# Optimization experiments

Measured on AMD Instinct MI355X. Metric: run time of the kernel, lower is better.

## Reference

```python
import jax, jax.numpy as jnp
import numpy as np

NUM_HEADS = 8

B, N, M = 2, 10000, 320000
QD = KD = HD = 256


def setup_inputs() -> dict:
    key = jax.random.key(0)
    k1, k2, k3, k4, k5 = jax.random.split(key, 5)
    x_q = jax.random.normal(k1, (B, N, QD), dtype=jnp.float32)
    x_k = jax.random.normal(k2, (B, N, KD), dtype=jnp.float32)
    mask = jax.random.randint(k3, (2, M), 0, N, dtype=jnp.int64)
    # xavier_uniform: limit = sqrt(6/(fan_in+fan_out))
    lim_q = float(np.sqrt(6.0 / (QD + HD)))
    lim_k = float(np.sqrt(6.0 / (KD + HD)))
    w_q = jax.random.uniform(k4, (QD, HD), minval=-lim_q, maxval=lim_q, dtype=jnp.float32)
    w_k = jax.random.uniform(k5, (KD, HD), minval=-lim_k, maxval=lim_k, dtype=jnp.float32)
    return {"x_q": x_q, "x_k": x_k, "mask": mask, "w_q": w_q, "w_k": w_k}


def reference(x_q, x_k, mask, w_q, w_k):
    b, n, _ = x_q.shape
    m = mask.shape[1]
    d = w_q.shape[1]          # hidden_dim
    h = NUM_HEADS
    dh = d // h
    q = x_q @ w_q             # (b, n, d)
    k = x_k @ w_k             # (b, n, d)
    # edge gather + elementwise multiply
    prod = q[:, mask[0], :] * k[:, mask[1], :]            # (b, m, d)
    # head buffer is i // (d/h): contiguous blocks -> reshape-sum
    a = prod.reshape(b, m, h, dh).sum(axis=-1)            # (b, m, h)
    a = a / jnp.sqrt(jnp.float32(w_k.shape[0]))           # / sqrt(key_dim)
    # segment softmax over destination index = mask[1 - reduce_dim], reduce_dim=1 -> mask[0]
    idx = mask[0]
    a = a - a.max()                                       # global max, as in source
    e = jnp.exp(a)                                        # (b, m, h)
    seg = jnp.zeros((b, n, h), e.dtype).at[:, idx, :].add(e)
    return e / (seg[:, idx, :] + 1e-16)
```

## Files before the change

kernel.cpp:

```cpp
#include <hip/hip_runtime.h>
#include <hip/hip_bf16.h>
#include <hip/hip_fp16.h>

#define DHID 256
#define NHEAD 8
#define BATCH 2
#define PAD 96

typedef _Float16 h8 __attribute__((ext_vector_type(8)));
typedef _Float16 h2 __attribute__((ext_vector_type(2)));
typedef float f4 __attribute__((ext_vector_type(4)));
typedef int i2 __attribute__((ext_vector_type(2)));

__global__ __launch_bounds__(256) void prep_kernel(
    const float* __restrict__ Wq, const float* __restrict__ Wk,
    _Float16* __restrict__ Wfq, _Float16* __restrict__ Wfk,
    int* __restrict__ cnt, int N)
{
    if (blockIdx.z == 2) {
        const int gid = (blockIdx.y * 8 + blockIdx.x) * 256
                      + threadIdx.y * 32 + threadIdx.x;
        if (gid < N) cnt[gid] = 0;
        return;
    }
    const float* W = blockIdx.z ? Wk : Wq;
    _Float16* Wf   = blockIdx.z ? Wfk : Wfq;
    __shared__ float tile[32][33];
    const int tx = threadIdx.x;
    const int ty = threadIdx.y;
    const int n0 = blockIdx.x * 32;
    const int k0 = blockIdx.y * 32;
#pragma unroll
    for (int j = 0; j < 32; j += 8)
        tile[ty + j][tx] = W[(size_t)(k0 + ty + j) * DHID + n0 + tx];
    __syncthreads();
#pragma unroll
    for (int j = 0; j < 32; j += 8) {
        const int n = n0 + ty + j;
        const int k = k0 + tx;
        const size_t u = ((size_t)(n >> 4) * 32 + (k >> 3)) * 16 + (n & 15);
        Wf[u * 8 + (k & 7)] = (_Float16)tile[tx][ty + j];
    }
}

__global__ __launch_bounds__(256, 4) void gemm_mfma(
    const float* __restrict__ Xq, const float* __restrict__ Xk,
    const _Float16* __restrict__ Wfq, const _Float16* __restrict__ Wfk,
    _Float16* __restrict__ Qh, _Float16* __restrict__ Kh,
    const int* __restrict__ mask, int* __restrict__ cnt, int* __restrict__ sde,
    int nx, int Mrows, int M, int N)
{
    const int t = threadIdx.x;
    if ((int)blockIdx.x >= nx) {
        const int sb = ((int)blockIdx.x - nx) + (blockIdx.z ? 64 : 0);
        for (int e = sb * 256 + t; e < M; e += 128 * 256) {
            int s = mask[e];
            int r = atomicAdd(&cnt[s], 1);
            if (r < PAD) {
                i2 v; v[0] = mask[M + e]; v[1] = e;
                *(i2*)(sde + ((size_t)s * PAD + r) * 2) = v;
            }
        }
        return;
    }

    const float* X     = blockIdx.z ? Xk : Xq;
    const _Float16* Wf = blockIdx.z ? Wfk : Wfq;
    _Float16* C        = blockIdx.z ? Kh : Qh;

    const int lane = t & 63;
    const int wave = t >> 6;
    const int quad = lane >> 4;
    const int l16  = lane & 15;
    const int rowBase = blockIdx.x * 64;
    int arow = rowBase + wave * 16 + l16;
    if (arow >= Mrows) arow = Mrows - 1;

    h8 af[8];
#pragma unroll
    for (int kc = 0; kc < 8; ++kc) {
        const float* p = X + (size_t)arow * DHID + (kc * 4 + quad) * 8;
        f4 v0 = *(const f4*)p;
        f4 v1 = *(const f4*)(p + 4);
        h8 hv;
        hv[0]=(_Float16)v0[0]; hv[1]=(_Float16)v0[1]; hv[2]=(_Float16)v0[2]; hv[3]=(_Float16)v0[3];
        hv[4]=(_Float16)v1[0]; hv[5]=(_Float16)v1[1]; hv[6]=(_Float16)v1[2]; hv[7]=(_Float16)v1[3];
        af[kc] = hv;
    }

#pragma unroll 1
    for (int ct64 = 0; ct64 < 4; ++ct64) {
        f4 acc[4] = {{0,0,0,0},{0,0,0,0},{0,0,0,0},{0,0,0,0}};
#pragma unroll
        for (int kc = 0; kc < 8; ++kc) {
#pragma unroll
            for (int ct = 0; ct < 4; ++ct) {
                const h8 bf = *(const h8*)(Wf +
                    (((size_t)(ct64 * 4 + ct) * 32 + kc * 4 + quad) * 16 + l16) * 8);
                acc[ct] = __builtin_amdgcn_mfma_f32_16x16x32_f16(af[kc], bf, acc[ct], 0, 0, 0);
            }
        }
#pragma unroll
        for (int ct = 0; ct < 4; ++ct) {
#pragma unroll
            for (int r = 0; r < 4; ++r) {
                int grow = rowBase + wave * 16 + quad * 4 + r;
                if (grow < Mrows) {
                    int bb = grow >= N;
                    int nn = grow - (bb ? N : 0);
                    C[((size_t)nn * 2 + bb) * DHID + ct64 * 64 + ct * 16 + l16]
                        = (_Float16)acc[ct][r];
                }
            }
        }
    }
}

__global__ __launch_bounds__(256, 8) void edge_kernel(
    const _Float16* __restrict__ Qh, const _Float16* __restrict__ Kh,
    const int* __restrict__ cnt, const int* __restrict__ sde,
    float* __restrict__ out, int M, int N)
{
    __shared__ _Float16 evs[4][PAD][2][NHEAD];
    const int lane = threadIdx.x & 63;
    const int wave = threadIdx.x >> 6;
    const int c    = lane & 31;
    const int half = lane >> 5;
    const int h    = c >> 2;
    const int src  = blockIdx.x * 4 + wave;
    if (src >= N) return;
    int deg = cnt[src];
    if (deg > PAD) deg = PAD;
    if (deg == 0) return;
    const size_t base = (size_t)src * PAD;

    int dstv = 0, eidv = 0;
    if (lane < deg) {
        i2 v = *(const i2*)(sde + (base + lane) * 2);
        dstv = v[0]; eidv = v[1];
    }

    const _Float16* Qrow = Qh + (size_t)src * 2 * DHID;
    const h8 q0 = *(const h8*)(Qrow + c * 8);
    const h8 q1 = *(const h8*)(Qrow + DHID + c * 8);

    float seg0 = 0.f, seg1 = 0.f;
    for (int it = 0; it < deg; it += 8) {
        int pl[4], dd[4];
#pragma unroll
        for (int p = 0; p < 4; ++p) {
            pl[p] = it + p * 2 + half;
            if (it < 64) {
                dd[p] = __shfl(dstv, pl[p]);
            } else {
                int sc = pl[p] < deg ? pl[p] : deg - 1;
                dd[p] = sde[(base + sc) * 2];
            }
        }
        h8 k0v[4], k1v[4];
#pragma unroll
        for (int p = 0; p < 4; ++p) {
            const _Float16* Krow = Kh + (size_t)dd[p] * 2 * DHID;
            k0v[p] = *(const h8*)(Krow + c * 8);
            k1v[p] = *(const h8*)(Krow + DHID + c * 8);
        }
#pragma unroll
        for (int p = 0; p < 4; ++p) {
            float s0 = 0.f, s1 = 0.f;
#if __has_builtin(__builtin_amdgcn_fdot2)
#pragma unroll
            for (int u = 0; u < 4; ++u) {
                h2 a0, b0, a1, b1;
                a0[0] = q0[2*u];      a0[1] = q0[2*u+1];
                b0[0] = k0v[p][2*u];  b0[1] = k0v[p][2*u+1];
                a1[0] = q1[2*u];      a1[1] = q1[2*u+1];
                b1[0] = k1v[p][2*u];  b1[1] = k1v[p][2*u+1];
                s0 = __builtin_amdgcn_fdot2(a0, b0, s0, false);
                s1 = __builtin_amdgcn_fdot2(a1, b1, s1, false);
            }
#else
#pragma unroll
            for (int u = 0; u < 8; ++u) {
                s0 += (float)q0[u] * (float)k0v[p][u];
                s1 += (float)q1[u] * (float)k1v[p][u];
            }
#endif
            s0 += __shfl_xor(s0, 1); s0 += __shfl_xor(s0, 2);
            s1 += __shfl_xor(s1, 1); s1 += __shfl_xor(s1, 2);
            if ((c & 3) == 0 && pl[p] < deg) {
                _Float16 e0 = (_Float16)expf(s0 * 0.0625f);
                _Float16 e1 = (_Float16)expf(s1 * 0.0625f);
                evs[wave][pl[p]][0][h] = e0;
                evs[wave][pl[p]][1][h] = e1;
                seg0 += (float)e0; seg1 += (float)e1;
            }
        }
    }

    seg0 += __shfl_xor(seg0, 32);
    seg1 += __shfl_xor(seg1, 32);
    const float r0 = __builtin_amdgcn_rcpf(seg0 + 1e-16f);
    const float r1 = __builtin_amdgcn_rcpf(seg1 + 1e-16f);

    for (int it = 0; it < deg; it += 8) {
        int pl[4], ee[4];
#pragma unroll
        for (int p = 0; p < 4; ++p) {
            pl[p] = it + p * 2 + half;
            if (it < 64) {
                ee[p] = __shfl(eidv, pl[p]);
            } else {
                int sc = pl[p] < deg ? pl[p] : deg - 1;
                ee[p] = sde[(base + sc) * 2 + 1];
            }
        }
#pragma unroll
        for (int p = 0; p < 4; ++p) {
            if ((c & 3) == 0 && pl[p] < deg) {
                float v0 = (float)evs[wave][pl[p]][0][h] * r0;
                float v1 = (float)evs[wave][pl[p]][1][h] * r1;
                __builtin_nontemporal_store(v0, &out[(size_t)ee[p] * NHEAD + h]);
                __builtin_nontemporal_store(v1,
                    &out[(size_t)M * NHEAD + (size_t)ee[p] * NHEAD + h]);
            }
        }
    }
}

extern "C" void kernel_launch(void* const* d_in, const int* in_sizes, int n_in,
                              void* d_out, int out_size, void* d_ws, size_t ws_size,
                              hipStream_t stream) {
    const float* x_q  = (const float*)d_in[0];
    const float* x_k  = (const float*)d_in[1];
    const int*   mask = (const int*)d_in[2];
    const float* w_q  = (const float*)d_in[3];
    const float* w_k  = (const float*)d_in[4];
    float* out = (float*)d_out;

    const int M = in_sizes[2] / 2;
    const int N = in_sizes[0] / (BATCH * DHID);
    const int Mrows = BATCH * N;

    _Float16* Qh  = (_Float16*)d_ws;
    _Float16* Kh  = Qh  + (size_t)Mrows * DHID;
    _Float16* Wfq = Kh  + (size_t)Mrows * DHID;
    _Float16* Wfk = Wfq + (size_t)DHID * DHID;
    int*      cnt = (int*)(Wfk + (size_t)DHID * DHID);
    int*      sde = cnt + N;

    prep_kernel<<<dim3(DHID / 32, DHID / 32, 3), dim3(32, 8), 0, stream>>>(
        w_q, w_k, Wfq, Wfk, cnt, N);

    const int nx = (Mrows + 63) / 64;
    gemm_mfma<<<dim3(nx + 64, 1, 2), 256, 0, stream>>>(
        x_q, x_k, Wfq, Wfk, Qh, Kh, mask, cnt, sde, nx, Mrows, M, N);

    edge_kernel<<<dim3((N + 3) / 4), 256, 0, stream>>>(
        Qh, Kh, cnt, sde, out, M, N);
}
```

Before: 171.6 us.

## Stage swizzled weight tiles in LDS with double buffering in projection GEMM

```diff
diff --git a/kernel.cpp b/kernel.cpp
--- a/kernel.cpp
+++ b/kernel.cpp
@@ -38,12 +38,13 @@
     for (int j = 0; j < 32; j += 8) {
         const int n = n0 + ty + j;
         const int k = k0 + tx;
-        const size_t u = ((size_t)(n >> 4) * 32 + (k >> 3)) * 16 + (n & 15);
-        Wf[u * 8 + (k & 7)] = (_Float16)tile[tx][ty + j];
-    }
-}
-
-__global__ __launch_bounds__(256, 4) void gemm_mfma(
+        const int ct64 = n >> 6, nl = n & 63, c = k >> 3, jj = k & 7;
+        Wf[(size_t)ct64 * 16384 + nl * 256 + ((c ^ (nl & 7)) << 3) + jj]
+            = (_Float16)tile[tx][ty + j];
+    }
+}
+
+__global__ __launch_bounds__(256, 2) void gemm_mfma(
     const float* __restrict__ Xq, const float* __restrict__ Xk,
     const _Float16* __restrict__ Wfq, const _Float16* __restrict__ Wfk,
     _Float16* __restrict__ Qh, _Float16* __restrict__ Kh,
@@ -68,6 +69,8 @@
     const _Float16* Wf = blockIdx.z ? Wfk : Wfq;
     _Float16* C        = blockIdx.z ? Kh : Qh;
 
+    __shared__ _Float16 Bs[2][16384];
+
     const int lane = t & 63;
     const int wave = t >> 6;
     const int quad = lane >> 4;
@@ -75,6 +78,24 @@
     const int rowBase = blockIdx.x * 64;
     int arow = rowBase + wave * 16 + l16;
     if (arow >= Mrows) arow = Mrows - 1;
+
+    auto stageB = [&](int ct64, int buf) {
+#pragma unroll
+        for (int i = 0; i < 8; ++i) {
+            const int ci = i * 4 + wave;
+            const _Float16* src = Wf + (size_t)ct64 * 16384 + ci * 512 + lane * 8;
+            _Float16* dst = &Bs[buf][ci * 512];
+#if __has_builtin(__builtin_amdgcn_global_load_lds)
+            __builtin_amdgcn_global_load_lds(
+                (__attribute__((address_space(1))) void*)src,
+                (__attribute__((address_space(3))) void*)dst, 16, 0, 0);
+#else
+            *(h8*)(dst + lane * 8) = *(const h8*)src;
+#endif
+        }
+    };
+
+    stageB(0, 0);
 
     h8 af[8];
 #pragma unroll
@@ -88,18 +109,25 @@
         af[kc] = hv;
     }
 
-#pragma unroll 1
+    __syncthreads();
+
+#pragma unroll
     for (int ct64 = 0; ct64 < 4; ++ct64) {
+        const int cur = ct64 & 1;
+        if (ct64 < 3) stageB(ct64 + 1, cur ^ 1);
+
         f4 acc[4] = {{0,0,0,0},{0,0,0,0},{0,0,0,0},{0,0,0,0}};
 #pragma unroll
         for (int kc = 0; kc < 8; ++kc) {
 #pragma unroll
             for (int ct = 0; ct < 4; ++ct) {
-                const h8 bf = *(const h8*)(Wf +
-                    (((size_t)(ct64 * 4 + ct) * 32 + kc * 4 + quad) * 16 + l16) * 8);
-                acc[ct] = __builtin_amdgcn_mfma_f32_16x16x32_f16(af[kc], bf, acc[ct], 0, 0, 0);
-            }
-        }
+                int bn = ct * 16 + l16;
+                int bc = (kc * 4 + quad) ^ (bn & 7);
+                h8 bfrag = *(const h8*)&Bs[cur][bn * 256 + bc * 8];
+                acc[ct] = __builtin_amdgcn_mfma_f32_16x16x32_f16(af[kc], bfrag, acc[ct], 0, 0, 0);
+            }
+        }
+
 #pragma unroll
         for (int ct = 0; ct < 4; ++ct) {
 #pragma unroll
@@ -113,6 +141,7 @@
                 }
             }
         }
+        __syncthreads();
     }
 }
 
@@ -188,8 +217,8 @@
             s0 += __shfl_xor(s0, 1); s0 += __shfl_xor(s0, 2);
             s1 += __shfl_xor(s1, 1); s1 += __shfl_xor(s1, 2);
             if ((c & 3) == 0 && pl[p] < deg) {
-                _Float16 e0 = (_Float16)expf(s0 * 0.0625f);
-                _Float16 e1 = (_Float16)expf(s1 * 0.0625f);
+                _Float16 e0 = (_Float16)__expf(s0 * 0.0625f);
+                _Float16 e1 = (_Float16)__expf(s1 * 0.0625f);
                 evs[wave][pl[p]][0][h] = e0;
                 evs[wave][pl[p]][1][h] = e1;
                 seg0 += (float)e0; seg1 += (float)e1;
```

New measurement: 167.0 us. -2.6%, faster.
